# Performance work log

Hardware: AMD Instinct MI355X
Metric: run time of the kernel (lower is better)

## Reference

```python
import jax, jax.numpy as jnp
import numpy as np

H = 4096
W = 4096
N_CELLS = H * W
ITERATIONS = 16


def setup_inputs() -> dict:
    key = jax.random.key(0)
    k1, k2 = jax.random.split(key)
    runoff = jax.random.uniform(k1, (H, W), dtype=jnp.float32)
    # each cell's downstream receiver cell (flat index into H*W grid)
    flow_idx = jax.random.randint(k2, (N_CELLS,), 0, N_CELLS, dtype=jnp.int32)
    return {
        "runoff_generated": runoff,
        "flow_direction_indices": flow_idx,
        "iterations": ITERATIONS,
    }


def reference(runoff_generated, flow_direction_indices, iterations):
    h, w = runoff_generated.shape
    current = runoff_generated.reshape(-1)   # (N,)
    accumulated = current                      # clone of initial flow

    def step(carry, _):
        accum, cur = carry
        # scatter-add: every cell pushes its current flow downstream
        accum = accum.at[flow_direction_indices].add(cur)
        cur = accum - cur
        return (accum, cur), None

    (accumulated, _), _ = jax.lax.scan(step, (accumulated, current), None, length=iterations)
    return accumulated.reshape(h, w)
```

## Files before the change

kernel.cpp:

```cpp
#include <hip/hip_runtime.h>


#define N_CELLS (1 << 24)

#define BKT_BITS 14
#define NBKT (N_CELLS >> BKT_BITS)
#define DPB (1 << BKT_BITS)
#define BKT_MASK (DPB - 1)
#define IDX_MASK (N_CELLS - 1)
#define G1 256
#define EDGES_PER_WG (N_CELLS / G1)
#define BT 1024

typedef unsigned uv4 __attribute__((ext_vector_type(4)));
typedef float fv4 __attribute__((ext_vector_type(4)));
typedef unsigned long long u64;

__device__ __align__(16) unsigned g_T[2][NBKT * G1];
__device__ __align__(16) unsigned g_bktcnt[2][NBKT];
__device__ __align__(16) unsigned g_S[2][NBKT + 4];
__device__ __align__(16) uint2 g_rec[N_CELLS];
__device__ __align__(16) int g_idx2[N_CELLS];
__device__ __align__(16) int g_idx4[N_CELLS];
__device__ __align__(16) float gB1[N_CELLS];
__device__ __align__(16) float gB2[N_CELLS];
__device__ __align__(16) float gB3[N_CELLS];
__device__ __align__(16) float gH[N_CELLS];

__global__ void compose_idx(const int* __restrict__ ext, int mode) {
    const int* __restrict__ a = mode ? g_idx2 : ext;
    int* __restrict__ o = mode ? g_idx4 : g_idx2;
    int i = (blockIdx.x * 256 + threadIdx.x) * 4;
    int4 v = *reinterpret_cast<const int4*>(a + i);
    int4 r;
    r.x = a[v.x & IDX_MASK];
    r.y = a[v.y & IDX_MASK];
    r.z = a[v.z & IDX_MASK];
    r.w = a[v.w & IDX_MASK];
    *reinterpret_cast<int4*>(o + i) = r;
}

__global__ void __launch_bounds__(BT) b1_count(const int* __restrict__ ext, int set) {
    const int* __restrict__ idx = set ? g_idx4 : ext;
    __shared__ unsigned h[NBKT];
    int t = threadIdx.x;
    h[t] = 0u;
    __syncthreads();
    const uv4* p = reinterpret_cast<const uv4*>(idx) + (size_t)blockIdx.x * (EDGES_PER_WG / 4);
    for (int k = 0; k < EDGES_PER_WG / 4 / BT; ++k) {
        uv4 v = __builtin_nontemporal_load(&p[k * BT + t]);
        atomicAdd(&h[(v.x & IDX_MASK) >> BKT_BITS], 1u);
        atomicAdd(&h[(v.y & IDX_MASK) >> BKT_BITS], 1u);
        atomicAdd(&h[(v.z & IDX_MASK) >> BKT_BITS], 1u);
        atomicAdd(&h[(v.w & IDX_MASK) >> BKT_BITS], 1u);
    }
    __syncthreads();
    g_T[set][(size_t)t * G1 + blockIdx.x] = h[t];
}

__global__ void s1_sums(int set) {
    __shared__ unsigned sd[256];
    int t = threadIdx.x;
    sd[t] = g_T[set][(size_t)blockIdx.x * G1 + t];
    __syncthreads();
    for (int off = 128; off > 0; off >>= 1) {
        if (t < off) sd[t] += sd[t + off];
        __syncthreads();
    }
    if (t == 0) g_bktcnt[set][blockIdx.x] = sd[0];
}

__global__ void s2_scan(int set) {
    __shared__ unsigned s[256];
    int t = threadIdx.x;
    uint4 v = reinterpret_cast<const uint4*>(g_bktcnt[set])[t];
    unsigned local = v.x + v.y + v.z + v.w;
    s[t] = local;
    __syncthreads();
    for (int off = 1; off < 256; off <<= 1) {
        unsigned add = (t >= off) ? s[t - off] : 0u;
        __syncthreads();
        s[t] += add;
        __syncthreads();
    }
    unsigned run = s[t] - local;
    uint4 o;
    o.x = run; run += v.x;
    o.y = run; run += v.y;
    o.z = run; run += v.z;
    o.w = run;
    reinterpret_cast<uint4*>(g_S[set])[t] = o;
    if (t == 0) g_S[set][NBKT] = (unsigned)N_CELLS;
}

__global__ void s3_offsets(int set) {
    __shared__ unsigned s[256];
    int t = threadIdx.x;
    unsigned v = g_T[set][(size_t)blockIdx.x * G1 + t];
    s[t] = v;
    __syncthreads();
    for (int off = 1; off < 256; off <<= 1) {
        unsigned add = (t >= off) ? s[t - off] : 0u;
        __syncthreads();
        s[t] += add;
        __syncthreads();
    }
    g_T[set][(size_t)blockIdx.x * G1 + t] = g_S[set][blockIdx.x] + s[t] - v;
}

__device__ __forceinline__ float* sel_buf(int which, const float* r, float* dout) {
    switch (which) {
        case 0: return (float*)r;
        case 1: return gB1;
        case 2: return gB2;
        case 3: return gB3;
        case 4: return gH;
        default: return dout;
    }
}

__global__ void __launch_bounds__(BT) route_op(const float* __restrict__ rin,
                                               float* __restrict__ dout,
                                               const int* __restrict__ ext,
                                               int ct_sel, int set) {
    const int* __restrict__ idx = set ? g_idx4 : ext;
    const float* __restrict__ ct = sel_buf(ct_sel, rin, dout);
    __shared__ unsigned cur[NBKT];
    int t = threadIdx.x;
    cur[t] = g_T[set][(size_t)t * G1 + blockIdx.x];
    __syncthreads();
    const uv4* ip = reinterpret_cast<const uv4*>(idx) + (size_t)blockIdx.x * (EDGES_PER_WG / 4);
    const fv4* cp = reinterpret_cast<const fv4*>(ct) + (size_t)blockIdx.x * (EDGES_PER_WG / 4);
    for (int k = 0; k < EDGES_PER_WG / 4 / BT; ++k) {
        uv4 v = __builtin_nontemporal_load(&ip[k * BT + t]);
        fv4 c = __builtin_nontemporal_load(&cp[k * BT + t]);
        unsigned e, p;
        e = v.x & IDX_MASK; p = atomicAdd(&cur[e >> BKT_BITS], 1u) & IDX_MASK;
        g_rec[p] = make_uint2(__float_as_uint(c.x), e & BKT_MASK);
        e = v.y & IDX_MASK; p = atomicAdd(&cur[e >> BKT_BITS], 1u) & IDX_MASK;
        g_rec[p] = make_uint2(__float_as_uint(c.y), e & BKT_MASK);
        e = v.z & IDX_MASK; p = atomicAdd(&cur[e >> BKT_BITS], 1u) & IDX_MASK;
        g_rec[p] = make_uint2(__float_as_uint(c.z), e & BKT_MASK);
        e = v.w & IDX_MASK; p = atomicAdd(&cur[e >> BKT_BITS], 1u) & IDX_MASK;
        g_rec[p] = make_uint2(__float_as_uint(c.w), e & BKT_MASK);
    }
}

__global__ void __launch_bounds__(512) acc_op(const float* __restrict__ rin,
                                              float* __restrict__ dout,
                                              int out_sel, int set, int fuse,
                                              float a0, float a1, float a2, float a3) {
    __shared__ float acc[DPB];
    int t = threadIdx.x;
    unsigned b = blockIdx.x;
    float* __restrict__ out = sel_buf(out_sel, rin, dout);
    unsigned base = g_S[set][b];
    unsigned end = g_S[set][b + 1];
    if (end > (unsigned)N_CELLS) end = (unsigned)N_CELLS;
    if (base > end) base = end;
    fv4* acc4 = reinterpret_cast<fv4*>(acc);
    fv4 z = (fv4)(0.0f);
    for (int k = 0; k < DPB / 4 / 512; ++k) acc4[k * 512 + t] = z;
    __syncthreads();
    const u64* __restrict__ rec = reinterpret_cast<const u64*>(g_rec);
    unsigned e = base + t;
    for (; e + 1536 < end; e += 2048) {
        u64 q0 = __builtin_nontemporal_load(&rec[e]);
        u64 q1 = __builtin_nontemporal_load(&rec[e + 512]);
        u64 q2 = __builtin_nontemporal_load(&rec[e + 1024]);
        u64 q3 = __builtin_nontemporal_load(&rec[e + 1536]);
        atomicAdd(&acc[(unsigned)(q0 >> 32) & BKT_MASK], __uint_as_float((unsigned)q0));
        atomicAdd(&acc[(unsigned)(q1 >> 32) & BKT_MASK], __uint_as_float((unsigned)q1));
        atomicAdd(&acc[(unsigned)(q2 >> 32) & BKT_MASK], __uint_as_float((unsigned)q2));
        atomicAdd(&acc[(unsigned)(q3 >> 32) & BKT_MASK], __uint_as_float((unsigned)q3));
    }
    for (; e < end; e += 512) {
        u64 q = __builtin_nontemporal_load(&rec[e]);
        atomicAdd(&acc[(unsigned)(q >> 32) & BKT_MASK], __uint_as_float((unsigned)q));
    }
    __syncthreads();
    size_t rowbase = (size_t)b * (DPB / 4);
    fv4* out4 = reinterpret_cast<fv4*>(out) + rowbase;
    if (fuse) {
        const fv4* r4 = reinterpret_cast<const fv4*>(rin) + rowbase;
        const fv4* p1 = reinterpret_cast<const fv4*>(gB1) + rowbase;
        const fv4* p2 = reinterpret_cast<const fv4*>(gB2) + rowbase;
        const fv4* p3 = reinterpret_cast<const fv4*>(gB3) + rowbase;
        for (int k = 0; k < DPB / 4 / 512; ++k) {
            int j = k * 512 + t;
            fv4 a = acc4[j];
            fv4 x = __builtin_nontemporal_load(&r4[j]);
            fv4 y = __builtin_nontemporal_load(&p1[j]);
            fv4 u = __builtin_nontemporal_load(&p2[j]);
            fv4 w = __builtin_nontemporal_load(&p3[j]);
            a += a0 * x + a1 * y + a2 * u + a3 * w;
            __builtin_nontemporal_store(a, &out4[j]);
        }
    } else {
        for (int k = 0; k < DPB / 4 / 512; ++k) {
            int j = k * 512 + t;
            __builtin_nontemporal_store(acc4[j], &out4[j]);
        }
    }
}

extern "C" void kernel_launch(void* const* d_in, const int* in_sizes, int n_in,
                              void* d_out, int out_size, void* d_ws, size_t ws_size,
                              hipStream_t stream) {
    const int* idx = (const int*)d_in[1];
    const float* r = (const float*)d_in[0];
    float* out = (float*)d_out;

    b1_count<<<G1, BT, 0, stream>>>(idx, 0);
    s1_sums<<<NBKT, 256, 0, stream>>>(0);
    s2_scan<<<1, 256, 0, stream>>>(0);
    s3_offsets<<<NBKT, 256, 0, stream>>>(0);

    compose_idx<<<N_CELLS / 4 / 256, 256, 0, stream>>>(idx, 0);
    compose_idx<<<N_CELLS / 4 / 256, 256, 0, stream>>>(idx, 1);
    b1_count<<<G1, BT, 0, stream>>>(idx, 1);
    s1_sums<<<NBKT, 256, 0, stream>>>(1);
    s2_scan<<<1, 256, 0, stream>>>(1);
    s3_offsets<<<NBKT, 256, 0, stream>>>(1);

    route_op<<<G1, BT, 0, stream>>>(r, out, idx, 0, 0);
    acc_op<<<NBKT, 512, 0, stream>>>(r, out, 1, 0, 0, 0.f, 0.f, 0.f, 0.f);
    route_op<<<G1, BT, 0, stream>>>(r, out, idx, 1, 0);
    acc_op<<<NBKT, 512, 0, stream>>>(r, out, 2, 0, 0, 0.f, 0.f, 0.f, 0.f);
    route_op<<<G1, BT, 0, stream>>>(r, out, idx, 2, 0);
    acc_op<<<NBKT, 512, 0, stream>>>(r, out, 3, 0, 0, 0.f, 0.f, 0.f, 0.f);

    route_op<<<G1, BT, 0, stream>>>(r, out, idx, 0, 1);
    acc_op<<<NBKT, 512, 0, stream>>>(r, out, 4, 1, 1, 91.f, 14.f, 15.f, 1.f);
    route_op<<<G1, BT, 0, stream>>>(r, out, idx, 4, 1);
    acc_op<<<NBKT, 512, 0, stream>>>(r, out, 5, 1, 1, 495.f, 220.f, 286.f, 78.f);
    route_op<<<G1, BT, 0, stream>>>(r, out, idx, 5, 1);
    acc_op<<<NBKT, 512, 0, stream>>>(r, out, 4, 1, 1, 210.f, 252.f, 462.f, 330.f);
    route_op<<<G1, BT, 0, stream>>>(r, out, idx, 4, 1);
    acc_op<<<NBKT, 512, 0, stream>>>(r, out, 5, 1, 1, 1.f, 8.f, 36.f, 84.f);
}
```

Before: 3.133 ms.

## Replace random-gather index composition with bucketed route/gather/scatter passes

The direct composition idx2[i]=idx[idx[i]] performs fully random 4-byte gathers over a 64MB array. It is replaced by a multi-pass bucket sort: count destinations per bucket and chunk, scan the counts into offsets, route (source, offset) records into buckets, gather each bucket's values from a shared-memory window, then scatter the results back through a per-chunk window. The goal is to turn random global reads into coalesced, LDS-local accesses. The cost is several extra kernel launches and extra passes over a 128MB record buffer, and the scatter kernel runs a serial per-thread loop.

```diff
diff --git a/kernel.cpp b/kernel.cpp
--- a/kernel.cpp
+++ b/kernel.cpp
@@ -12,6 +12,9 @@
 #define EDGES_PER_WG (N_CELLS / G1)
 #define BT 1024
 
+#define CCH 1024
+#define CCHSZ (N_CELLS / CCH)
+
 typedef unsigned uv4 __attribute__((ext_vector_type(4)));
 typedef float fv4 __attribute__((ext_vector_type(4)));
 typedef unsigned long long u64;
@@ -20,6 +23,10 @@
 __device__ __align__(16) unsigned g_bktcnt[2][NBKT];
 __device__ __align__(16) unsigned g_S[2][NBKT + 4];
 __device__ __align__(16) uint2 g_rec[N_CELLS];
+__device__ __align__(16) unsigned g_C[NBKT * CCH];
+__device__ __align__(16) unsigned g_O[NBKT * CCH];
+__device__ __align__(16) unsigned g_CB[NBKT];
+__device__ __align__(16) unsigned g_CS[NBKT + 4];
 __device__ __align__(16) int g_idx2[N_CELLS];
 __device__ __align__(16) int g_idx4[N_CELLS];
 __device__ __align__(16) float gB1[N_CELLS];
@@ -27,18 +34,135 @@
 __device__ __align__(16) float gB3[N_CELLS];
 __device__ __align__(16) float gH[N_CELLS];
 
-__global__ void compose_idx(const int* __restrict__ ext, int mode) {
+
+__global__ void __launch_bounds__(BT) cmp_cnt(const int* __restrict__ ext, int mode) {
     const int* __restrict__ a = mode ? g_idx2 : ext;
+    __shared__ unsigned h[NBKT];
+    int t = threadIdx.x;
+    h[t] = 0u;
+    __syncthreads();
+    const uv4* p = reinterpret_cast<const uv4*>(a) + (size_t)blockIdx.x * (CCHSZ / 4);
+    for (int k = 0; k < CCHSZ / 4 / BT; ++k) {
+        uv4 v = __builtin_nontemporal_load(&p[k * BT + t]);
+        atomicAdd(&h[(v.x & IDX_MASK) >> BKT_BITS], 1u);
+        atomicAdd(&h[(v.y & IDX_MASK) >> BKT_BITS], 1u);
+        atomicAdd(&h[(v.z & IDX_MASK) >> BKT_BITS], 1u);
+        atomicAdd(&h[(v.w & IDX_MASK) >> BKT_BITS], 1u);
+    }
+    __syncthreads();
+    g_C[(size_t)t * CCH + blockIdx.x] = h[t];
+}
+
+__global__ void cmp_s1() {
+    __shared__ unsigned sd[256];
+    int t = threadIdx.x;
+    uint4 v = reinterpret_cast<const uint4*>(g_C + (size_t)blockIdx.x * CCH)[t];
+    sd[t] = v.x + v.y + v.z + v.w;
+    __syncthreads();
+    for (int off = 128; off > 0; off >>= 1) {
+        if (t < off) sd[t] += sd[t + off];
+        __syncthreads();
+    }
+    if (t == 0) g_CB[blockIdx.x] = sd[0];
+}
+
+__global__ void cmp_s2() {
+    __shared__ unsigned s[256];
+    int t = threadIdx.x;
+    uint4 v = reinterpret_cast<const uint4*>(g_CB)[t];
+    unsigned local = v.x + v.y + v.z + v.w;
+    s[t] = local;
+    __syncthreads();
+    for (int off = 1; off < 256; off <<= 1) {
+        unsigned add = (t >= off) ? s[t - off] : 0u;
+        __syncthreads();
+        s[t] += add;
+        __syncthreads();
+    }
+    unsigned run = s[t] - local;
+    uint4 o;
+    o.x = run; run += v.x;
+    o.y = run; run += v.y;
+    o.z = run; run += v.z;
+    o.w = run;
+    reinterpret_cast<uint4*>(g_CS)[t] = o;
+    if (t == 0) g_CS[NBKT] = (unsigned)N_CELLS;
+}
+
+__global__ void __launch_bounds__(BT) cmp_s3() {
+    __shared__ unsigned s[BT];
+    int t = threadIdx.x;
+    unsigned c = g_C[(size_t)blockIdx.x * CCH + t];
+    s[t] = c;
+    __syncthreads();
+    for (int off = 1; off < BT; off <<= 1) {
+        unsigned add = (t >= off) ? s[t - off] : 0u;
+        __syncthreads();
+        s[t] += add;
+        __syncthreads();
+    }
+    g_O[(size_t)blockIdx.x * CCH + t] = g_CS[blockIdx.x] + s[t] - c;
+}
+
+__global__ void __launch_bounds__(BT) cmp_route(const int* __restrict__ ext, int mode) {
+    const int* __restrict__ a = mode ? g_idx2 : ext;
+    __shared__ unsigned cur[NBKT];
+    int t = threadIdx.x;
+    cur[t] = g_O[(size_t)t * CCH + blockIdx.x];
+    __syncthreads();
+    const uv4* p = reinterpret_cast<const uv4*>(a) + (size_t)blockIdx.x * (CCHSZ / 4);
+    unsigned base_i = blockIdx.x * CCHSZ;
+    for (int k = 0; k < CCHSZ / 4 / BT; ++k) {
+        uv4 v = __builtin_nontemporal_load(&p[k * BT + t]);
+        unsigned i0 = base_i + (k * BT + t) * 4;
+        unsigned e, pos;
+        e = v.x & IDX_MASK; pos = atomicAdd(&cur[e >> BKT_BITS], 1u) & IDX_MASK;
+        g_rec[pos] = make_uint2(i0, e & BKT_MASK);
+        e = v.y & IDX_MASK; pos = atomicAdd(&cur[e >> BKT_BITS], 1u) & IDX_MASK;
+        g_rec[pos] = make_uint2(i0 + 1, e & BKT_MASK);
+        e = v.z & IDX_MASK; pos = atomicAdd(&cur[e >> BKT_BITS], 1u) & IDX_MASK;
+        g_rec[pos] = make_uint2(i0 + 2, e & BKT_MASK);
+        e = v.w & IDX_MASK; pos = atomicAdd(&cur[e >> BKT_BITS], 1u) & IDX_MASK;
+        g_rec[pos] = make_uint2(i0 + 3, e & BKT_MASK);
+    }
+}
+
+__global__ void __launch_bounds__(BT) cmp_gather(const int* __restrict__ ext, int mode) {
+    const int* __restrict__ a = mode ? g_idx2 : ext;
+    __shared__ unsigned lds[DPB];
+    int t = threadIdx.x;
+    unsigned b = blockIdx.x;
+    for (int j = t; j < DPB; j += BT) lds[j] = (unsigned)a[(size_t)b * DPB + j];
+    __syncthreads();
+    unsigned start = g_CS[b];
+    unsigned end = g_CS[b + 1];
+    if (end > (unsigned)N_CELLS) end = (unsigned)N_CELLS;
+    if (start > end) start = end;
+    for (unsigned e = start + t; e < end; e += BT) {
+        uint2 q = g_rec[e];
+        g_rec[e] = make_uint2(q.x, lds[q.y & BKT_MASK]);
+    }
+}
+
+__global__ void __launch_bounds__(BT) cmp_scatter(int mode) {
     int* __restrict__ o = mode ? g_idx4 : g_idx2;
-    int i = (blockIdx.x * 256 + threadIdx.x) * 4;
-    int4 v = *reinterpret_cast<const int4*>(a + i);
-    int4 r;
-    r.x = a[v.x & IDX_MASK];
-    r.y = a[v.y & IDX_MASK];
-    r.z = a[v.z & IDX_MASK];
-    r.w = a[v.w & IDX_MASK];
-    *reinterpret_cast<int4*>(o + i) = r;
-}
+    __shared__ unsigned win[DPB];
+    int t = threadIdx.x;
+    unsigned w = blockIdx.x;
+    for (int j = t; j < DPB; j += BT) win[j] = 0u;
+    __syncthreads();
+    unsigned start = g_O[(size_t)t * CCH + w];
+    unsigned end = (w == CCH - 1) ? g_CS[t + 1] : g_O[(size_t)t * CCH + w + 1];
+    if (start > (unsigned)N_CELLS) start = (unsigned)N_CELLS;
+    if (end > (unsigned)N_CELLS) end = (unsigned)N_CELLS;
+    for (unsigned e = start; e < end; ++e) {
+        uint2 q = g_rec[e];
+        win[q.x & BKT_MASK] = q.y;
+    }
+    __syncthreads();
+    for (int j = t; j < DPB; j += BT) o[(size_t)w * DPB + j] = (int)win[j];
+}
+
 
 __global__ void __launch_bounds__(BT) b1_count(const int* __restrict__ ext, int set) {
     const int* __restrict__ idx = set ? g_idx4 : ext;
@@ -216,8 +340,22 @@
     s2_scan<<<1, 256, 0, stream>>>(0);
     s3_offsets<<<NBKT, 256, 0, stream>>>(0);
 
-    compose_idx<<<N_CELLS / 4 / 256, 256, 0, stream>>>(idx, 0);
-    compose_idx<<<N_CELLS / 4 / 256, 256, 0, stream>>>(idx, 1);
+    cmp_cnt<<<CCH, BT, 0, stream>>>(idx, 0);
+    cmp_s1<<<NBKT, 256, 0, stream>>>();
+    cmp_s2<<<1, 256, 0, stream>>>();
+    cmp_s3<<<NBKT, BT, 0, stream>>>();
+    cmp_route<<<CCH, BT, 0, stream>>>(idx, 0);
+    cmp_gather<<<NBKT, BT, 0, stream>>>(idx, 0);
+    cmp_scatter<<<CCH, BT, 0, stream>>>(0);
+
+    cmp_cnt<<<CCH, BT, 0, stream>>>(idx, 1);
+    cmp_s1<<<NBKT, 256, 0, stream>>>();
+    cmp_s2<<<1, 256, 0, stream>>>();
+    cmp_s3<<<NBKT, BT, 0, stream>>>();
+    cmp_route<<<CCH, BT, 0, stream>>>(idx, 1);
+    cmp_gather<<<NBKT, BT, 0, stream>>>(idx, 1);
+    cmp_scatter<<<CCH, BT, 0, stream>>>(1);
+
     b1_count<<<G1, BT, 0, stream>>>(idx, 1);
     s1_sums<<<NBKT, 256, 0, stream>>>(1);
     s2_scan<<<1, 256, 0, stream>>>(1);
```

After: 3.409 ms. 8.8% more time.

## Batch scatter records per bucket into 32-byte writes with padded segments

Applied to the files above, without the earlier changes.

The routing kernel now runs 1024 single-wavefront workgroups. Each one stages records per destination bucket in shared memory and writes them out as aligned groups of four (32 bytes), replacing scattered 8-byte stores. Per-workgroup bucket counts are padded to multiples of four, so the record buffer doubles in size and the counting and offset kernels are resized to match. The aim is to cut write-transaction overhead on the scatter. In exchange, each element now goes through a claim/barrier loop, and occupancy drops with 64-thread workgroups and scalar loads, which may serialize the route phase.

```diff
diff --git a/kernel.cpp b/kernel.cpp
--- a/kernel.cpp
+++ b/kernel.cpp
@@ -8,24 +8,28 @@
 #define DPB (1 << BKT_BITS)
 #define BKT_MASK (DPB - 1)
 #define IDX_MASK (N_CELLS - 1)
-#define G1 256
-#define EDGES_PER_WG (N_CELLS / G1)
-#define BT 1024
+
+#define NW 1024
+#define EPW (N_CELLS / NW)
+#define RECN (1u << 25)
+#define REC_MASK (RECN - 1u)
 
 typedef unsigned uv4 __attribute__((ext_vector_type(4)));
 typedef float fv4 __attribute__((ext_vector_type(4)));
 typedef unsigned long long u64;
 
-__device__ __align__(16) unsigned g_T[2][NBKT * G1];
+__device__ __align__(16) unsigned g_T[2][NBKT * NW];
 __device__ __align__(16) unsigned g_bktcnt[2][NBKT];
 __device__ __align__(16) unsigned g_S[2][NBKT + 4];
-__device__ __align__(16) uint2 g_rec[N_CELLS];
+__device__ __align__(16) uint2 g_rec[RECN];
 __device__ __align__(16) int g_idx2[N_CELLS];
 __device__ __align__(16) int g_idx4[N_CELLS];
 __device__ __align__(16) float gB1[N_CELLS];
 __device__ __align__(16) float gB2[N_CELLS];
 __device__ __align__(16) float gB3[N_CELLS];
 __device__ __align__(16) float gH[N_CELLS];
+
+__device__ __forceinline__ unsigned pad4(unsigned c) { return (c + 3u) & ~3u; }
 
 __global__ void compose_idx(const int* __restrict__ ext, int mode) {
     const int* __restrict__ a = mode ? g_idx2 : ext;
@@ -40,28 +44,29 @@
     *reinterpret_cast<int4*>(o + i) = r;
 }
 
-__global__ void __launch_bounds__(BT) b1_count(const int* __restrict__ ext, int set) {
+__global__ void __launch_bounds__(64) b1_count(const int* __restrict__ ext, int set) {
     const int* __restrict__ idx = set ? g_idx4 : ext;
     __shared__ unsigned h[NBKT];
     int t = threadIdx.x;
-    h[t] = 0u;
-    __syncthreads();
-    const uv4* p = reinterpret_cast<const uv4*>(idx) + (size_t)blockIdx.x * (EDGES_PER_WG / 4);
-    for (int k = 0; k < EDGES_PER_WG / 4 / BT; ++k) {
-        uv4 v = __builtin_nontemporal_load(&p[k * BT + t]);
+    for (int b = t; b < NBKT; b += 64) h[b] = 0u;
+    __syncthreads();
+    const uv4* p = reinterpret_cast<const uv4*>(idx) + (size_t)blockIdx.x * (EPW / 4);
+    for (int k = 0; k < EPW / 4 / 64; ++k) {
+        uv4 v = __builtin_nontemporal_load(&p[k * 64 + t]);
         atomicAdd(&h[(v.x & IDX_MASK) >> BKT_BITS], 1u);
         atomicAdd(&h[(v.y & IDX_MASK) >> BKT_BITS], 1u);
         atomicAdd(&h[(v.z & IDX_MASK) >> BKT_BITS], 1u);
         atomicAdd(&h[(v.w & IDX_MASK) >> BKT_BITS], 1u);
     }
     __syncthreads();
-    g_T[set][(size_t)t * G1 + blockIdx.x] = h[t];
+    for (int b = t; b < NBKT; b += 64) g_T[set][(size_t)b * NW + blockIdx.x] = h[b];
 }
 
 __global__ void s1_sums(int set) {
     __shared__ unsigned sd[256];
     int t = threadIdx.x;
-    sd[t] = g_T[set][(size_t)blockIdx.x * G1 + t];
+    uint4 v = reinterpret_cast<const uint4*>(g_T[set] + (size_t)blockIdx.x * NW)[t];
+    sd[t] = pad4(v.x) + pad4(v.y) + pad4(v.z) + pad4(v.w);
     __syncthreads();
     for (int off = 128; off > 0; off >>= 1) {
         if (t < off) sd[t] += sd[t + off];
@@ -90,22 +95,22 @@
     o.z = run; run += v.z;
     o.w = run;
     reinterpret_cast<uint4*>(g_S[set])[t] = o;
-    if (t == 0) g_S[set][NBKT] = (unsigned)N_CELLS;
-}
-
-__global__ void s3_offsets(int set) {
-    __shared__ unsigned s[256];
-    int t = threadIdx.x;
-    unsigned v = g_T[set][(size_t)blockIdx.x * G1 + t];
-    s[t] = v;
-    __syncthreads();
-    for (int off = 1; off < 256; off <<= 1) {
+    if (t == 255) g_S[set][NBKT] = run + v.w;
+}
+
+__global__ void __launch_bounds__(1024) s3_offsets(int set) {
+    __shared__ unsigned s[NW];
+    int t = threadIdx.x;
+    unsigned c = pad4(g_T[set][(size_t)blockIdx.x * NW + t]);
+    s[t] = c;
+    __syncthreads();
+    for (int off = 1; off < NW; off <<= 1) {
         unsigned add = (t >= off) ? s[t - off] : 0u;
         __syncthreads();
         s[t] += add;
         __syncthreads();
     }
-    g_T[set][(size_t)blockIdx.x * G1 + t] = g_S[set][blockIdx.x] + s[t] - v;
+    g_T[set][(size_t)blockIdx.x * NW + t] = g_S[set][blockIdx.x] + s[t] - c;
 }
 
 __device__ __forceinline__ float* sel_buf(int which, const float* r, float* dout) {
@@ -119,30 +124,60 @@
     }
 }
 
-__global__ void __launch_bounds__(BT) route_op(const float* __restrict__ rin,
+__global__ void __launch_bounds__(64) lg_route(const float* __restrict__ rin,
                                                float* __restrict__ dout,
                                                const int* __restrict__ ext,
                                                int ct_sel, int set) {
     const int* __restrict__ idx = set ? g_idx4 : ext;
     const float* __restrict__ ct = sel_buf(ct_sel, rin, dout);
-    __shared__ unsigned cur[NBKT];
-    int t = threadIdx.x;
-    cur[t] = g_T[set][(size_t)t * G1 + blockIdx.x];
-    __syncthreads();
-    const uv4* ip = reinterpret_cast<const uv4*>(idx) + (size_t)blockIdx.x * (EDGES_PER_WG / 4);
-    const fv4* cp = reinterpret_cast<const fv4*>(ct) + (size_t)blockIdx.x * (EDGES_PER_WG / 4);
-    for (int k = 0; k < EDGES_PER_WG / 4 / BT; ++k) {
-        uv4 v = __builtin_nontemporal_load(&ip[k * BT + t]);
-        fv4 c = __builtin_nontemporal_load(&cp[k * BT + t]);
-        unsigned e, p;
-        e = v.x & IDX_MASK; p = atomicAdd(&cur[e >> BKT_BITS], 1u) & IDX_MASK;
-        g_rec[p] = make_uint2(__float_as_uint(c.x), e & BKT_MASK);
-        e = v.y & IDX_MASK; p = atomicAdd(&cur[e >> BKT_BITS], 1u) & IDX_MASK;
-        g_rec[p] = make_uint2(__float_as_uint(c.y), e & BKT_MASK);
-        e = v.z & IDX_MASK; p = atomicAdd(&cur[e >> BKT_BITS], 1u) & IDX_MASK;
-        g_rec[p] = make_uint2(__float_as_uint(c.z), e & BKT_MASK);
-        e = v.w & IDX_MASK; p = atomicAdd(&cur[e >> BKT_BITS], 1u) & IDX_MASK;
-        g_rec[p] = make_uint2(__float_as_uint(c.w), e & BKT_MASK);
+    __shared__ unsigned curA[NBKT];
+    __shared__ unsigned claim[NBKT];
+    __shared__ uint2 buf[NBKT][4];
+    int t = threadIdx.x;
+    unsigned wg = blockIdx.x;
+    for (int b = t; b < NBKT; b += 64) curA[b] = g_T[set][(size_t)b * NW + wg];
+    __syncthreads();
+    size_t ebase = (size_t)wg * EPW;
+    for (int k = 0; k < EPW / 64; ++k) {
+        size_t e = ebase + (size_t)k * 64 + t;
+        unsigned d = ((unsigned)__builtin_nontemporal_load(&idx[e])) & IDX_MASK;
+        float v = __builtin_nontemporal_load(&ct[e]);
+        unsigned b = d >> BKT_BITS;
+        bool active = true;
+        while (__any(active)) {
+            if (active) claim[b] = (unsigned)t;
+            __syncthreads();
+            bool win = active && (claim[b] == (unsigned)t);
+            if (win) {
+                unsigned pos = curA[b];
+                curA[b] = pos + 1u;
+                unsigned slot = pos & 3u;
+                buf[b][slot] = make_uint2(__float_as_uint(v), d & BKT_MASK);
+                if (slot == 3u) {
+                    uint2 r0 = buf[b][0], r1 = buf[b][1];
+                    uint2 r2 = buf[b][2], r3 = buf[b][3];
+                    uint4* dst4 = reinterpret_cast<uint4*>(&g_rec[(pos - 3u) & REC_MASK]);
+                    dst4[0] = make_uint4(r0.x, r0.y, r1.x, r1.y);
+                    dst4[1] = make_uint4(r2.x, r2.y, r3.x, r3.y);
+                }
+                active = false;
+            }
+            __syncthreads();
+        }
+    }
+    __syncthreads();
+    for (int b = t; b < NBKT; b += 64) {
+        unsigned pos = curA[b];
+        unsigned tl = pos & 3u;
+        if (tl) {
+            uint2 z = make_uint2(0u, 0u);
+            uint2 r0 = buf[b][0];
+            uint2 r1 = (tl > 1u) ? buf[b][1] : z;
+            uint2 r2 = (tl > 2u) ? buf[b][2] : z;
+            uint4* dst4 = reinterpret_cast<uint4*>(&g_rec[(pos - tl) & REC_MASK]);
+            dst4[0] = make_uint4(r0.x, r0.y, r1.x, r1.y);
+            dst4[1] = make_uint4(r2.x, r2.y, 0u, 0u);
+        }
     }
 }
 
@@ -156,7 +191,7 @@
     float* __restrict__ out = sel_buf(out_sel, rin, dout);
     unsigned base = g_S[set][b];
     unsigned end = g_S[set][b + 1];
-    if (end > (unsigned)N_CELLS) end = (unsigned)N_CELLS;
+    if (end > RECN) end = RECN;
     if (base > end) base = end;
     fv4* acc4 = reinterpret_cast<fv4*>(acc);
     fv4 z = (fv4)(0.0f);
@@ -211,31 +246,31 @@
     const float* r = (const float*)d_in[0];
     float* out = (float*)d_out;
 
-    b1_count<<<G1, BT, 0, stream>>>(idx, 0);
+    b1_count<<<NW, 64, 0, stream>>>(idx, 0);
     s1_sums<<<NBKT, 256, 0, stream>>>(0);
     s2_scan<<<1, 256, 0, stream>>>(0);
-    s3_offsets<<<NBKT, 256, 0, stream>>>(0);
+    s3_offsets<<<NBKT, 1024, 0, stream>>>(0);
 
     compose_idx<<<N_CELLS / 4 / 256, 256, 0, stream>>>(idx, 0);
     compose_idx<<<N_CELLS / 4 / 256, 256, 0, stream>>>(idx, 1);
-    b1_count<<<G1, BT, 0, stream>>>(idx, 1);
+    b1_count<<<NW, 64, 0, stream>>>(idx, 1);
     s1_sums<<<NBKT, 256, 0, stream>>>(1);
     s2_scan<<<1, 256, 0, stream>>>(1);
-    s3_offsets<<<NBKT, 256, 0, stream>>>(1);
-
-    route_op<<<G1, BT, 0, stream>>>(r, out, idx, 0, 0);
+    s3_offsets<<<NBKT, 1024, 0, stream>>>(1);
+
+    lg_route<<<NW, 64, 0, stream>>>(r, out, idx, 0, 0);
     acc_op<<<NBKT, 512, 0, stream>>>(r, out, 1, 0, 0, 0.f, 0.f, 0.f, 0.f);
-    route_op<<<G1, BT, 0, stream>>>(r, out, idx, 1, 0);
+    lg_route<<<NW, 64, 0, stream>>>(r, out, idx, 1, 0);
     acc_op<<<NBKT, 512, 0, stream>>>(r, out, 2, 0, 0, 0.f, 0.f, 0.f, 0.f);
-    route_op<<<G1, BT, 0, stream>>>(r, out, idx, 2, 0);
+    lg_route<<<NW, 64, 0, stream>>>(r, out, idx, 2, 0);
     acc_op<<<NBKT, 512, 0, stream>>>(r, out, 3, 0, 0, 0.f, 0.f, 0.f, 0.f);
 
-    route_op<<<G1, BT, 0, stream>>>(r, out, idx, 0, 1);
+    lg_route<<<NW, 64, 0, stream>>>(r, out, idx, 0, 1);
     acc_op<<<NBKT, 512, 0, stream>>>(r, out, 4, 1, 1, 91.f, 14.f, 15.f, 1.f);
-    route_op<<<G1, BT, 0, stream>>>(r, out, idx, 4, 1);
+    lg_route<<<NW, 64, 0, stream>>>(r, out, idx, 4, 1);
     acc_op<<<NBKT, 512, 0, stream>>>(r, out, 5, 1, 1, 495.f, 220.f, 286.f, 78.f);
-    route_op<<<G1, BT, 0, stream>>>(r, out, idx, 5, 1);
+    lg_route<<<NW, 64, 0, stream>>>(r, out, idx, 5, 1);
     acc_op<<<NBKT, 512, 0, stream>>>(r, out, 4, 1, 1, 210.f, 252.f, 462.f, 330.f);
-    route_op<<<G1, BT, 0, stream>>>(r, out, idx, 4, 1);
+    lg_route<<<NW, 64, 0, stream>>>(r, out, idx, 4, 1);
     acc_op<<<NBKT, 512, 0, stream>>>(r, out, 5, 1, 1, 1.f, 8.f, 36.f, 84.f);
 }
```

New measurement: 3.794 ms. 21.1% more time.

## Co-schedule index composition and histogramming with routing passes in fused launches

Applied to the files above, without the earlier changes.

Index composition (idx∘idx, then idx²∘idx²) and the histogram of the composed index no longer run as their own launches. They are merged into the early routing passes with block-index dispatch, so independent memory-bound work shares one grid and fills idle compute units. The routing and histogram grid goes from 256 workgroups of 1024 threads to 512 of 512, which changes occupancy and per-workgroup work. In exchange the kernels are more heterogeneous, shared-memory use differs between the branches, and the block interleaving could unbalance the load.

```diff
diff --git a/kernel.cpp b/kernel.cpp
--- a/kernel.cpp
+++ b/kernel.cpp
@@ -8,9 +8,10 @@
 #define DPB (1 << BKT_BITS)
 #define BKT_MASK (DPB - 1)
 #define IDX_MASK (N_CELLS - 1)
-#define G1 256
-#define EDGES_PER_WG (N_CELLS / G1)
-#define BT 1024
+#define G1 512
+#define BT 512
+#define EPW (N_CELLS / G1)
+#define CBLK 8192
 
 typedef unsigned uv4 __attribute__((ext_vector_type(4)));
 typedef float fv4 __attribute__((ext_vector_type(4)));
@@ -27,87 +28,6 @@
 __device__ __align__(16) float gB3[N_CELLS];
 __device__ __align__(16) float gH[N_CELLS];
 
-__global__ void compose_idx(const int* __restrict__ ext, int mode) {
-    const int* __restrict__ a = mode ? g_idx2 : ext;
-    int* __restrict__ o = mode ? g_idx4 : g_idx2;
-    int i = (blockIdx.x * 256 + threadIdx.x) * 4;
-    int4 v = *reinterpret_cast<const int4*>(a + i);
-    int4 r;
-    r.x = a[v.x & IDX_MASK];
-    r.y = a[v.y & IDX_MASK];
-    r.z = a[v.z & IDX_MASK];
-    r.w = a[v.w & IDX_MASK];
-    *reinterpret_cast<int4*>(o + i) = r;
-}
-
-__global__ void __launch_bounds__(BT) b1_count(const int* __restrict__ ext, int set) {
-    const int* __restrict__ idx = set ? g_idx4 : ext;
-    __shared__ unsigned h[NBKT];
-    int t = threadIdx.x;
-    h[t] = 0u;
-    __syncthreads();
-    const uv4* p = reinterpret_cast<const uv4*>(idx) + (size_t)blockIdx.x * (EDGES_PER_WG / 4);
-    for (int k = 0; k < EDGES_PER_WG / 4 / BT; ++k) {
-        uv4 v = __builtin_nontemporal_load(&p[k * BT + t]);
-        atomicAdd(&h[(v.x & IDX_MASK) >> BKT_BITS], 1u);
-        atomicAdd(&h[(v.y & IDX_MASK) >> BKT_BITS], 1u);
-        atomicAdd(&h[(v.z & IDX_MASK) >> BKT_BITS], 1u);
-        atomicAdd(&h[(v.w & IDX_MASK) >> BKT_BITS], 1u);
-    }
-    __syncthreads();
-    g_T[set][(size_t)t * G1 + blockIdx.x] = h[t];
-}
-
-__global__ void s1_sums(int set) {
-    __shared__ unsigned sd[256];
-    int t = threadIdx.x;
-    sd[t] = g_T[set][(size_t)blockIdx.x * G1 + t];
-    __syncthreads();
-    for (int off = 128; off > 0; off >>= 1) {
-        if (t < off) sd[t] += sd[t + off];
-        __syncthreads();
-    }
-    if (t == 0) g_bktcnt[set][blockIdx.x] = sd[0];
-}
-
-__global__ void s2_scan(int set) {
-    __shared__ unsigned s[256];
-    int t = threadIdx.x;
-    uint4 v = reinterpret_cast<const uint4*>(g_bktcnt[set])[t];
-    unsigned local = v.x + v.y + v.z + v.w;
-    s[t] = local;
-    __syncthreads();
-    for (int off = 1; off < 256; off <<= 1) {
-        unsigned add = (t >= off) ? s[t - off] : 0u;
-        __syncthreads();
-        s[t] += add;
-        __syncthreads();
-    }
-    unsigned run = s[t] - local;
-    uint4 o;
-    o.x = run; run += v.x;
-    o.y = run; run += v.y;
-    o.z = run; run += v.z;
-    o.w = run;
-    reinterpret_cast<uint4*>(g_S[set])[t] = o;
-    if (t == 0) g_S[set][NBKT] = (unsigned)N_CELLS;
-}
-
-__global__ void s3_offsets(int set) {
-    __shared__ unsigned s[256];
-    int t = threadIdx.x;
-    unsigned v = g_T[set][(size_t)blockIdx.x * G1 + t];
-    s[t] = v;
-    __syncthreads();
-    for (int off = 1; off < 256; off <<= 1) {
-        unsigned add = (t >= off) ? s[t - off] : 0u;
-        __syncthreads();
-        s[t] += add;
-        __syncthreads();
-    }
-    g_T[set][(size_t)blockIdx.x * G1 + t] = g_S[set][blockIdx.x] + s[t] - v;
-}
-
 __device__ __forceinline__ float* sel_buf(int which, const float* r, float* dout) {
     switch (which) {
         case 0: return (float*)r;
@@ -119,19 +39,30 @@
     }
 }
 
-__global__ void __launch_bounds__(BT) route_op(const float* __restrict__ rin,
-                                               float* __restrict__ dout,
-                                               const int* __restrict__ ext,
-                                               int ct_sel, int set) {
-    const int* __restrict__ idx = set ? g_idx4 : ext;
-    const float* __restrict__ ct = sel_buf(ct_sel, rin, dout);
-    __shared__ unsigned cur[NBKT];
-    int t = threadIdx.x;
-    cur[t] = g_T[set][(size_t)t * G1 + blockIdx.x];
-    __syncthreads();
-    const uv4* ip = reinterpret_cast<const uv4*>(idx) + (size_t)blockIdx.x * (EDGES_PER_WG / 4);
-    const fv4* cp = reinterpret_cast<const fv4*>(ct) + (size_t)blockIdx.x * (EDGES_PER_WG / 4);
-    for (int k = 0; k < EDGES_PER_WG / 4 / BT; ++k) {
+
+__device__ __forceinline__ void dev_compose(const int* __restrict__ ext, int mode,
+                                            unsigned cid, int t) {
+    const int* __restrict__ a = mode ? g_idx2 : ext;
+    int* __restrict__ o = mode ? g_idx4 : g_idx2;
+    size_t i = ((size_t)cid * BT + t) * 4;
+    int4 v = *reinterpret_cast<const int4*>(a + i);
+    int4 r;
+    r.x = a[v.x & IDX_MASK];
+    r.y = a[v.y & IDX_MASK];
+    r.z = a[v.z & IDX_MASK];
+    r.w = a[v.w & IDX_MASK];
+    *reinterpret_cast<int4*>(o + i) = r;
+}
+
+__device__ __forceinline__ void dev_route(const float* __restrict__ ct,
+                                          const int* __restrict__ idx,
+                                          unsigned* cur, unsigned wg, int t, int set) {
+    cur[t] = g_T[set][(size_t)t * G1 + wg];
+    cur[t + 512] = g_T[set][(size_t)(t + 512) * G1 + wg];
+    __syncthreads();
+    const uv4* ip = reinterpret_cast<const uv4*>(idx) + (size_t)wg * (EPW / 4);
+    const fv4* cp = reinterpret_cast<const fv4*>(ct) + (size_t)wg * (EPW / 4);
+    for (int k = 0; k < EPW / 4 / BT; ++k) {
         uv4 v = __builtin_nontemporal_load(&ip[k * BT + t]);
         fv4 c = __builtin_nontemporal_load(&cp[k * BT + t]);
         unsigned e, p;
@@ -144,6 +75,121 @@
         e = v.w & IDX_MASK; p = atomicAdd(&cur[e >> BKT_BITS], 1u) & IDX_MASK;
         g_rec[p] = make_uint2(__float_as_uint(c.w), e & BKT_MASK);
     }
+}
+
+__device__ __forceinline__ void dev_b1(const int* __restrict__ idx,
+                                       unsigned* h, unsigned wg, int t, int set) {
+    h[t] = 0u; h[t + 512] = 0u;
+    __syncthreads();
+    const uv4* p = reinterpret_cast<const uv4*>(idx) + (size_t)wg * (EPW / 4);
+    for (int k = 0; k < EPW / 4 / BT; ++k) {
+        uv4 v = __builtin_nontemporal_load(&p[k * BT + t]);
+        atomicAdd(&h[(v.x & IDX_MASK) >> BKT_BITS], 1u);
+        atomicAdd(&h[(v.y & IDX_MASK) >> BKT_BITS], 1u);
+        atomicAdd(&h[(v.z & IDX_MASK) >> BKT_BITS], 1u);
+        atomicAdd(&h[(v.w & IDX_MASK) >> BKT_BITS], 1u);
+    }
+    __syncthreads();
+    g_T[set][(size_t)t * G1 + wg] = h[t];
+    g_T[set][(size_t)(t + 512) * G1 + wg] = h[t + 512];
+}
+
+
+__global__ void __launch_bounds__(BT) k_b1(const int* __restrict__ ext, int set) {
+    __shared__ unsigned h[NBKT];
+    const int* __restrict__ idx = set ? g_idx4 : ext;
+    dev_b1(idx, h, blockIdx.x, threadIdx.x, set);
+}
+
+__global__ void __launch_bounds__(BT) k_route(const float* __restrict__ rin,
+                                              float* __restrict__ dout,
+                                              const int* __restrict__ ext,
+                                              int ct_sel, int set) {
+    __shared__ unsigned cur[NBKT];
+    const int* __restrict__ idx = set ? g_idx4 : ext;
+    const float* __restrict__ ct = sel_buf(ct_sel, rin, dout);
+    dev_route(ct, idx, cur, blockIdx.x, threadIdx.x, set);
+}
+
+__global__ void __launch_bounds__(BT) fat_cr(const float* __restrict__ rin,
+                                             float* __restrict__ dout,
+                                             const int* __restrict__ ext,
+                                             int mode, int ct_sel, int set) {
+    __shared__ unsigned cur[NBKT];
+    unsigned b = blockIdx.x;
+    unsigned q = b / 17u, rmd = b % 17u;
+    if (rmd == 16u) {
+        const int* __restrict__ idx = set ? g_idx4 : ext;
+        const float* __restrict__ ct = sel_buf(ct_sel, rin, dout);
+        dev_route(ct, idx, cur, q, threadIdx.x, set);
+    } else {
+        dev_compose(ext, mode, q * 16u + rmd, threadIdx.x);
+    }
+}
+
+__global__ void __launch_bounds__(BT) fat_br(const float* __restrict__ rin,
+                                             float* __restrict__ dout,
+                                             const int* __restrict__ ext,
+                                             int ct_sel) {
+    __shared__ unsigned lds[NBKT];
+    unsigned b = blockIdx.x;
+    if (b & 1u) {
+        const float* __restrict__ ct = sel_buf(ct_sel, rin, dout);
+        dev_route(ct, ext, lds, b >> 1, threadIdx.x, 0);
+    } else {
+        dev_b1(g_idx4, lds, b >> 1, threadIdx.x, 1);
+    }
+}
+
+__global__ void s1_sums(int set) {
+    __shared__ unsigned sd[256];
+    int t = threadIdx.x;
+    uint2 v = reinterpret_cast<const uint2*>(g_T[set] + (size_t)blockIdx.x * G1)[t];
+    sd[t] = v.x + v.y;
+    __syncthreads();
+    for (int off = 128; off > 0; off >>= 1) {
+        if (t < off) sd[t] += sd[t + off];
+        __syncthreads();
+    }
+    if (t == 0) g_bktcnt[set][blockIdx.x] = sd[0];
+}
+
+__global__ void s2_scan(int set) {
+    __shared__ unsigned s[256];
+    int t = threadIdx.x;
+    uint4 v = reinterpret_cast<const uint4*>(g_bktcnt[set])[t];
+    unsigned local = v.x + v.y + v.z + v.w;
+    s[t] = local;
+    __syncthreads();
+    for (int off = 1; off < 256; off <<= 1) {
+        unsigned add = (t >= off) ? s[t - off] : 0u;
+        __syncthreads();
+        s[t] += add;
+        __syncthreads();
+    }
+    unsigned run = s[t] - local;
+    uint4 o;
+    o.x = run; run += v.x;
+    o.y = run; run += v.y;
+    o.z = run; run += v.z;
+    o.w = run;
+    reinterpret_cast<uint4*>(g_S[set])[t] = o;
+    if (t == 0) g_S[set][NBKT] = (unsigned)N_CELLS;
+}
+
+__global__ void __launch_bounds__(BT) s3_offsets(int set) {
+    __shared__ unsigned s[G1];
+    int t = threadIdx.x;
+    unsigned v = g_T[set][(size_t)blockIdx.x * G1 + t];
+    s[t] = v;
+    __syncthreads();
+    for (int off = 1; off < G1; off <<= 1) {
+        unsigned add = (t >= off) ? s[t - off] : 0u;
+        __syncthreads();
+        s[t] += add;
+        __syncthreads();
+    }
+    g_T[set][(size_t)blockIdx.x * G1 + t] = g_S[set][blockIdx.x] + s[t] - v;
 }
 
 __global__ void __launch_bounds__(512) acc_op(const float* __restrict__ rin,
@@ -211,31 +257,27 @@
     const float* r = (const float*)d_in[0];
     float* out = (float*)d_out;
 
-    b1_count<<<G1, BT, 0, stream>>>(idx, 0);
+    k_b1<<<G1, BT, 0, stream>>>(idx, 0);
     s1_sums<<<NBKT, 256, 0, stream>>>(0);
     s2_scan<<<1, 256, 0, stream>>>(0);
-    s3_offsets<<<NBKT, 256, 0, stream>>>(0);
-
-    compose_idx<<<N_CELLS / 4 / 256, 256, 0, stream>>>(idx, 0);
-    compose_idx<<<N_CELLS / 4 / 256, 256, 0, stream>>>(idx, 1);
-    b1_count<<<G1, BT, 0, stream>>>(idx, 1);
+    s3_offsets<<<NBKT, BT, 0, stream>>>(0);
+
+    fat_cr<<<CBLK + G1, BT, 0, stream>>>(r, out, idx, 0, 0, 0);
+    acc_op<<<NBKT, 512, 0, stream>>>(r, out, 1, 0, 0, 0.f, 0.f, 0.f, 0.f);
+    fat_cr<<<CBLK + G1, BT, 0, stream>>>(r, out, idx, 1, 1, 0);
+    acc_op<<<NBKT, 512, 0, stream>>>(r, out, 2, 0, 0, 0.f, 0.f, 0.f, 0.f);
+    fat_br<<<2 * G1, BT, 0, stream>>>(r, out, idx, 2);
+    acc_op<<<NBKT, 512, 0, stream>>>(r, out, 3, 0, 0, 0.f, 0.f, 0.f, 0.f);
     s1_sums<<<NBKT, 256, 0, stream>>>(1);
     s2_scan<<<1, 256, 0, stream>>>(1);
-    s3_offsets<<<NBKT, 256, 0, stream>>>(1);
-
-    route_op<<<G1, BT, 0, stream>>>(r, out, idx, 0, 0);
-    acc_op<<<NBKT, 512, 0, stream>>>(r, out, 1, 0, 0, 0.f, 0.f, 0.f, 0.f);
-    route_op<<<G1, BT, 0, stream>>>(r, out, idx, 1, 0);
-    acc_op<<<NBKT, 512, 0, stream>>>(r, out, 2, 0, 0, 0.f, 0.f, 0.f, 0.f);
-    route_op<<<G1, BT, 0, stream>>>(r, out, idx, 2, 0);
-    acc_op<<<NBKT, 512, 0, stream>>>(r, out, 3, 0, 0, 0.f, 0.f, 0.f, 0.f);
-
-    route_op<<<G1, BT, 0, stream>>>(r, out, idx, 0, 1);
+    s3_offsets<<<NBKT, BT, 0, stream>>>(1);
+
+    k_route<<<G1, BT, 0, stream>>>(r, out, idx, 0, 1);
     acc_op<<<NBKT, 512, 0, stream>>>(r, out, 4, 1, 1, 91.f, 14.f, 15.f, 1.f);
-    route_op<<<G1, BT, 0, stream>>>(r, out, idx, 4, 1);
+    k_route<<<G1, BT, 0, stream>>>(r, out, idx, 4, 1);
     acc_op<<<NBKT, 512, 0, stream>>>(r, out, 5, 1, 1, 495.f, 220.f, 286.f, 78.f);
-    route_op<<<G1, BT, 0, stream>>>(r, out, idx, 5, 1);
+    k_route<<<G1, BT, 0, stream>>>(r, out, idx, 5, 1);
     acc_op<<<NBKT, 512, 0, stream>>>(r, out, 4, 1, 1, 210.f, 252.f, 462.f, 330.f);
-    route_op<<<G1, BT, 0, stream>>>(r, out, idx, 4, 1);
+    k_route<<<G1, BT, 0, stream>>>(r, out, idx, 4, 1);
     acc_op<<<NBKT, 512, 0, stream>>>(r, out, 5, 1, 1, 1.f, 8.f, 36.f, 84.f);
 }
```

After: 3.150 ms. No clear change (+0.5%).
